# Performance work log

Measured on AMD Instinct MI355X. Metric: run time of the kernel, lower is better.

## Reference

```python
import jax, jax.numpy as jnp
import numpy as np

N_BLOBS = 8
# blob_configs (static, from init_kwargs)
SIDE_RIGHT = np.array([1, 0, 1, 0, 1, 0, 1, 0], dtype=bool)  # right -> positions[:, :3]
START_Y = np.array([0.1, 0.2, 0.3, 0.4, 0.5, 0.6, 0.7, 0.8], dtype=np.float32)
START_X = np.array([0.8, 0.7, 0.6, 0.5, 0.4, 0.3, 0.2, 0.1], dtype=np.float32)
START_S = np.full(N_BLOBS, 0.05, dtype=np.float32)
A_MIN = np.full(N_BLOBS, 0.5, dtype=np.float32)
A_MAX = np.full(N_BLOBS, 2.0, dtype=np.float32)
EPS = 1e-6


def setup_inputs() -> dict:
    key = jax.random.key(0)
    ks = jax.random.split(key, 8)
    B, H = 256, 64
    return {
        "positions": jax.random.normal(ks[0], (B, 6), jnp.float32),
        "W1": jax.random.normal(ks[1], (N_BLOBS, 3, H), jnp.float32) * 0.1,
        "b1": jnp.zeros((N_BLOBS, H), jnp.float32),
        "W2": jax.random.normal(ks[2], (N_BLOBS, H, H), jnp.float32) * 0.1,
        "b2": jnp.zeros((N_BLOBS, H), jnp.float32),
        "W3": jax.random.normal(ks[3], (N_BLOBS, H, 5), jnp.float32) * 0.1,
        "b3": jnp.zeros((N_BLOBS, 5), jnp.float32),
        "target_size": 256,
        "blobs_scale_factor": jnp.ones((), jnp.float32),
    }


def _encode_all(positions, W1, b1, W2, b2, W3, b3):
    """Per-blob MLP over selected half of positions -> [N_BLOBS, B, 5] blob data."""
    side = jnp.asarray(SIDE_RIGHT)[:, None, None]  # [N,1,1]
    # right blobs use first 3 coords, left blobs use last 3
    pos = jnp.where(side, positions[None, :, :3], positions[None, :, 3:]) * 100.0  # [N,B,3]
    h = jax.nn.relu(jnp.einsum('nbi,nih->nbh', pos, W1) + b1[:, None, :])
    h = jax.nn.relu(jnp.einsum('nbh,nhk->nbk', h, W2) + b2[:, None, :])
    bd = jnp.einsum('nbh,nhk->nbk', h, W3) + b3[:, None, :]  # [N,B,5]
    y = jax.nn.sigmoid(bd[..., 0]) + jnp.asarray(START_Y)[:, None]
    x = jax.nn.sigmoid(bd[..., 1]) + jnp.asarray(START_X)[:, None]
    s = bd[..., 2] + jnp.asarray(START_S)[:, None]
    a = jnp.asarray(A_MIN)[:, None] + jax.nn.sigmoid(bd[..., 3]) * (jnp.asarray(A_MAX) - jnp.asarray(A_MIN))[:, None]
    th = jax.nn.sigmoid(bd[..., 4]) * jnp.pi
    return y, x, s, a, th  # each [N,B]


def _splat(y, x, s, a, th, T):
    """Elliptical gaussian splat for one blob: params [B] -> image [B,T,T]."""
    coords = (jnp.arange(T, dtype=jnp.float32) + 0.5) / T  # pixel centers in [0,1)
    dy = coords[None, :, None] - y[:, None, None]  # [B,T,1]
    dx = coords[None, None, :] - x[:, None, None]  # [B,1,T]
    c = jnp.cos(th)[:, None, None]
    sn = jnp.sin(th)[:, None, None]
    u = c * dy + sn * dx   # rotated coords [B,T,T]
    v = -sn * dy + c * dx
    sa = (s * a)[:, None, None] + EPS   # major sigma
    sb = (s / (a + EPS))[:, None, None] + EPS  # minor sigma
    return jnp.exp(-0.5 * ((u / sa) ** 2 + (v / sb) ** 2))


def reference(positions, W1, b1, W2, b2, W3, b3, target_size, blobs_scale_factor):
    y, x, s, a, th = _encode_all(positions, W1, b1, W2, b2, W3, b3)
    s = s * blobs_scale_factor
    B = positions.shape[0]
    img = jnp.zeros((B, target_size, target_size), positions.dtype)
    for i in range(N_BLOBS):  # small fixed blob count; sequential blend as in source
        cur = _splat(y[i], x[i], s[i], a[i], th[i], target_size)
        img = img * cur + cur  # mul then add with same blob image
    return img
```

## Files before the change

kernel.cpp:

```cpp
#include <hip/hip_runtime.h>
#include <math.h>

#define NBLOBS 8
#define HID    64
#define TSZ    256
#define BATCH  256
#define EPSV   1e-6f

#if __has_builtin(__builtin_amdgcn_exp2f)
#define FAST_EXP(x) __builtin_amdgcn_exp2f(x)
#define PRESCALE 0.8493218002880191f
#else
#define FAST_EXP(x) __expf(x)
#define PRESCALE 0.7071067811865476f
#endif

__device__ __forceinline__ float sigmoidf_(float x) {
    return 1.0f / (1.0f + __expf(-x));
}

__global__ __launch_bounds__(64) void encode_kernel(
    const float* __restrict__ positions,
    const float* __restrict__ W1,
    const float* __restrict__ b1,
    const float* __restrict__ W2,
    const float* __restrict__ b2,
    const float* __restrict__ W3,
    const float* __restrict__ b3,
    const float* __restrict__ scale_ptr,
    float* __restrict__ params)
{
    const int n   = blockIdx.x;
    const int tid = threadIdx.x;

    __shared__ float sW1[3 * HID];
    __shared__ float sB1[HID];
    __shared__ float sW2[HID * HID];
    __shared__ float sB2[HID];
    __shared__ float sW3[HID * 5];
    __shared__ float sB3[5];

    for (int i = tid; i < 3 * HID; i += 64) sW1[i] = W1[n * 3 * HID + i];
    for (int i = tid; i < HID; i += 64) {
        sB1[i] = b1[n * HID + i];
        sB2[i] = b2[n * HID + i];
    }
    {
        float4*       s4 = (float4*)sW2;
        const float4* g4 = (const float4*)(W2 + n * HID * HID);
        for (int i = tid; i < HID * HID / 4; i += 64) s4[i] = g4[i];
    }
    for (int i = tid; i < HID * 5; i += 64) sW3[i] = W3[n * HID * 5 + i];
    if (tid < 5) sB3[tid] = b3[n * 5 + tid];
    __syncthreads();

    const int b = blockIdx.y * 64 + tid;
    const int off = (n & 1) ? 3 : 0;
    const float p0 = positions[b * 6 + off + 0] * 100.0f;
    const float p1 = positions[b * 6 + off + 1] * 100.0f;
    const float p2 = positions[b * 6 + off + 2] * 100.0f;

    float h1[HID];
#pragma unroll
    for (int k = 0; k < HID; ++k) {
        float acc = sB1[k];
        acc = fmaf(p0, sW1[0 * HID + k], acc);
        acc = fmaf(p1, sW1[1 * HID + k], acc);
        acc = fmaf(p2, sW1[2 * HID + k], acc);
        h1[k] = fmaxf(acc, 0.0f);
    }

    float acc[HID];
#pragma unroll
    for (int k = 0; k < HID; ++k) acc[k] = sB2[k];
#pragma unroll
    for (int h = 0; h < HID; ++h) {
        const float xh = h1[h];
#pragma unroll
        for (int k4 = 0; k4 < HID / 4; ++k4) {
            const float4 w = *(const float4*)&sW2[h * HID + 4 * k4];
            acc[4 * k4 + 0] = fmaf(xh, w.x, acc[4 * k4 + 0]);
            acc[4 * k4 + 1] = fmaf(xh, w.y, acc[4 * k4 + 1]);
            acc[4 * k4 + 2] = fmaf(xh, w.z, acc[4 * k4 + 2]);
            acc[4 * k4 + 3] = fmaf(xh, w.w, acc[4 * k4 + 3]);
        }
    }
#pragma unroll
    for (int k = 0; k < HID; ++k) acc[k] = fmaxf(acc[k], 0.0f);

    float bd[5];
#pragma unroll
    for (int j = 0; j < 5; ++j) bd[j] = sB3[j];
#pragma unroll
    for (int h = 0; h < HID; ++h) {
        const float xh = acc[h];
#pragma unroll
        for (int j = 0; j < 5; ++j)
            bd[j] = fmaf(xh, sW3[h * 5 + j], bd[j]);
    }

    const float scale = scale_ptr[0];
    const float y  = sigmoidf_(bd[0]) + 0.1f * (float)(n + 1);
    const float x  = sigmoidf_(bd[1]) + 0.1f * (float)(8 - n);
    const float s  = (bd[2] + 0.05f) * scale;
    const float a  = 0.5f + sigmoidf_(bd[3]) * 1.5f;
    const float th = sigmoidf_(bd[4]) * 3.14159265358979323846f;

    float sn, c;
    sincosf(th, &sn, &c);

    const float sa = s * a + EPSV;
    const float sb = s / (a + EPSV) + EPSV;
    const float ia = PRESCALE / sa;
    const float ib = PRESCALE / sb;

    const float A = c * ia;
    const float B = sn * ia;
    const float C = -sn * ib;
    const float D = c * ib;

    const float M   = -2.0f * (A * B + C * D);
    const float Qx  = -(B * B + D * D);
    const float del = -(A * A + C * C);

    float* p = params + (n * BATCH + b) * 8;
    p[0] = x;
    p[1] = M;
    p[2] = Qx;
    p[3] = del;
    p[4] = -2.0f * y * del;
    p[5] = -y;
    p[6] = del * y * y;
    p[7] = 0.0f;
}

__global__ __launch_bounds__(256) void splat_kernel(
    const float* __restrict__ params,
    float* __restrict__ out)
{
    const int b = blockIdx.z;

    __shared__ float sp[NBLOBS * 8];
    if (threadIdx.x < NBLOBS * 8) {
        const int n = threadIdx.x >> 3;
        const int f = threadIdx.x & 7;
        sp[threadIdx.x] = params[(n * BATCH + b) * 8 + f];
    }
    __syncthreads();

    const int j  = blockIdx.x * 64 + (threadIdx.x & 63);
    const int r0 = blockIdx.y * 32 + (threadIdx.x >> 6) * 8;
    const float cj = ((float)j + 0.5f) * (1.0f / TSZ);

    float ci[8], ci2[8];
#pragma unroll
    for (int r = 0; r < 8; ++r) {
        ci[r]  = ((float)(r0 + r) + 0.5f) * (1.0f / TSZ);
        ci2[r] = ci[r] * ci[r];
    }

    float img[8];
#pragma unroll
    for (int r = 0; r < 8; ++r) img[r] = 0.0f;

#pragma unroll
    for (int n = 0; n < NBLOBS; ++n) {
        const float x    = sp[n * 8 + 0];
        const float M    = sp[n * 8 + 1];
        const float Qx   = sp[n * 8 + 2];
        const float del  = sp[n * 8 + 3];
        const float m2yd = sp[n * 8 + 4];
        const float negy = sp[n * 8 + 5];
        const float y2d  = sp[n * 8 + 6];

        const float dx  = cj - x;
        const float dx2 = dx * dx;
        const float e   = M * dx;
        const float b1c = e + m2yd;
        const float b0c = fmaf(negy, e, fmaf(Qx, dx2, y2d));

#pragma unroll
        for (int r = 0; r < 8; ++r) {
            const float t   = fmaf(ci2[r], del, fmaf(ci[r], b1c, b0c));
            const float cur = FAST_EXP(t);
            img[r] = fmaf(img[r], cur, cur);
        }
    }

    float* dst = out + (size_t)b * TSZ * TSZ + (size_t)r0 * TSZ + j;
#pragma unroll
    for (int r = 0; r < 8; ++r) dst[r * TSZ] = img[r];
}

extern "C" void kernel_launch(void* const* d_in, const int* in_sizes, int n_in,
                              void* d_out, int out_size, void* d_ws, size_t ws_size,
                              hipStream_t stream) {
    const float* positions = (const float*)d_in[0];
    const float* W1        = (const float*)d_in[1];
    const float* b1        = (const float*)d_in[2];
    const float* W2        = (const float*)d_in[3];
    const float* b2        = (const float*)d_in[4];
    const float* W3        = (const float*)d_in[5];
    const float* b3        = (const float*)d_in[6];
    const float* scale_ptr = (const float*)d_in[8];

    float* params = (float*)d_ws;
    float* out    = (float*)d_out;

    encode_kernel<<<dim3(NBLOBS, BATCH / 64), dim3(64), 0, stream>>>(
        positions, W1, b1, W2, b2, W3, b3, scale_ptr, params);

    splat_kernel<<<dim3(TSZ / 64, TSZ / 32, BATCH), dim3(256), 0, stream>>>(params, out);
}
```

Baseline: 127.7 us.

## Split encode MLP hidden dim across 4 lanes per sample and Horner-form splat exponent

```diff
diff --git a/kernel.cpp b/kernel.cpp
--- a/kernel.cpp
+++ b/kernel.cpp
@@ -54,7 +54,11 @@
     if (tid < 5) sB3[tid] = b3[n * 5 + tid];
     __syncthreads();
 
-    const int b = blockIdx.y * 64 + tid;
+    const int bl = tid & 15;
+    const int q  = tid >> 4;
+    const int b  = blockIdx.y * 16 + bl;
+    const int k0 = q * 16;
+
     const int off = (n & 1) ? 3 : 0;
     const float p0 = positions[b * 6 + off + 0] * 100.0f;
     const float p1 = positions[b * 6 + off + 1] * 100.0f;
@@ -70,33 +74,36 @@
         h1[k] = fmaxf(acc, 0.0f);
     }
 
-    float acc[HID];
-#pragma unroll
-    for (int k = 0; k < HID; ++k) acc[k] = sB2[k];
+    float acc[16];
+#pragma unroll
+    for (int k = 0; k < 16; ++k) acc[k] = sB2[k0 + k];
 #pragma unroll
     for (int h = 0; h < HID; ++h) {
         const float xh = h1[h];
 #pragma unroll
-        for (int k4 = 0; k4 < HID / 4; ++k4) {
-            const float4 w = *(const float4*)&sW2[h * HID + 4 * k4];
+        for (int k4 = 0; k4 < 4; ++k4) {
+            const float4 w = *(const float4*)&sW2[h * HID + k0 + 4 * k4];
             acc[4 * k4 + 0] = fmaf(xh, w.x, acc[4 * k4 + 0]);
             acc[4 * k4 + 1] = fmaf(xh, w.y, acc[4 * k4 + 1]);
             acc[4 * k4 + 2] = fmaf(xh, w.z, acc[4 * k4 + 2]);
             acc[4 * k4 + 3] = fmaf(xh, w.w, acc[4 * k4 + 3]);
         }
     }
-#pragma unroll
-    for (int k = 0; k < HID; ++k) acc[k] = fmaxf(acc[k], 0.0f);
 
     float bd[5];
 #pragma unroll
-    for (int j = 0; j < 5; ++j) bd[j] = sB3[j];
-#pragma unroll
-    for (int h = 0; h < HID; ++h) {
-        const float xh = acc[h];
+    for (int j = 0; j < 5; ++j) bd[j] = (q == 0) ? sB3[j] : 0.0f;
+#pragma unroll
+    for (int k = 0; k < 16; ++k) {
+        const float xh = fmaxf(acc[k], 0.0f);
 #pragma unroll
         for (int j = 0; j < 5; ++j)
-            bd[j] = fmaf(xh, sW3[h * 5 + j], bd[j]);
+            bd[j] = fmaf(xh, sW3[(k0 + k) * 5 + j], bd[j]);
+    }
+#pragma unroll
+    for (int j = 0; j < 5; ++j) {
+        bd[j] += __shfl_xor(bd[j], 16, 64);
+        bd[j] += __shfl_xor(bd[j], 32, 64);
     }
 
     const float scale = scale_ptr[0];
@@ -123,15 +130,11 @@
     const float Qx  = -(B * B + D * D);
     const float del = -(A * A + C * C);
 
-    float* p = params + (n * BATCH + b) * 8;
-    p[0] = x;
-    p[1] = M;
-    p[2] = Qx;
-    p[3] = del;
-    p[4] = -2.0f * y * del;
-    p[5] = -y;
-    p[6] = del * y * y;
-    p[7] = 0.0f;
+    if (q == 0) {
+        float4* p = (float4*)(params + (n * BATCH + b) * 8);
+        p[0] = make_float4(x, M, Qx, del);
+        p[1] = make_float4(-2.0f * y * del, -y, del * y * y, 0.0f);
+    }
 }
 
 __global__ __launch_bounds__(256) void splat_kernel(
@@ -152,12 +155,10 @@
     const int r0 = blockIdx.y * 32 + (threadIdx.x >> 6) * 8;
     const float cj = ((float)j + 0.5f) * (1.0f / TSZ);
 
-    float ci[8], ci2[8];
-#pragma unroll
-    for (int r = 0; r < 8; ++r) {
-        ci[r]  = ((float)(r0 + r) + 0.5f) * (1.0f / TSZ);
-        ci2[r] = ci[r] * ci[r];
-    }
+    float ci[8];
+#pragma unroll
+    for (int r = 0; r < 8; ++r)
+        ci[r] = ((float)(r0 + r) + 0.5f) * (1.0f / TSZ);
 
     float img[8];
 #pragma unroll
@@ -174,14 +175,13 @@
         const float y2d  = sp[n * 8 + 6];
 
         const float dx  = cj - x;
-        const float dx2 = dx * dx;
         const float e   = M * dx;
         const float b1c = e + m2yd;
-        const float b0c = fmaf(negy, e, fmaf(Qx, dx2, y2d));
+        const float b0c = fmaf(negy, e, fmaf(Qx, dx * dx, y2d));
 
 #pragma unroll
         for (int r = 0; r < 8; ++r) {
-            const float t   = fmaf(ci2[r], del, fmaf(ci[r], b1c, b0c));
+            const float t   = fmaf(ci[r], fmaf(ci[r], del, b1c), b0c);
             const float cur = FAST_EXP(t);
             img[r] = fmaf(img[r], cur, cur);
         }
@@ -207,7 +207,7 @@
     float* params = (float*)d_ws;
     float* out    = (float*)d_out;
 
-    encode_kernel<<<dim3(NBLOBS, BATCH / 64), dim3(64), 0, stream>>>(
+    encode_kernel<<<dim3(NBLOBS, BATCH / 16), dim3(64), 0, stream>>>(
         positions, W1, b1, W2, b2, W3, b3, scale_ptr, params);
 
     splat_kernel<<<dim3(TSZ / 64, TSZ / 32, BATCH), dim3(256), 0, stream>>>(params, out);
```

Result: faster. 117.6 us (median of 2 runs) (-7.9%).
